# Performance work log

Measured on AMD Instinct MI355X. Metric: run time of the kernel, lower is better.

The kernel has to match this reference:

```python
import jax, jax.numpy as jnp
import numpy as np

B, P, U = 512, 24, 24
IN_T, IN_I, IN_O = 768, 2048, 512
INI = 512            # ini_hidden_dim for all three input linears
H = 1000             # BiLSTM hidden; embed_d = 2*H
E = 2 * H            # embed_d = 2000
INIA = 512           # agg init_linear out dim
HA = 1000            # agg BiLSTM hidden


def _bilstm1(x, W, b):
    """Single-step bidirectional LSTM from zero initial state.
    x: [..., D], W: [2, 4H, D] (fwd/bwd stacked), b: [2, 4H] (b_ih+b_hh).
    With h0=c0=0: gates = x@W_ih^T + b; c = sigmoid(i)*tanh(g); h = sigmoid(o)*tanh(c).
    Returns [..., 2H] (fwd then bwd, matching torch bidirectional concat)."""
    g = jnp.einsum('...d,khd->...kh', x, W) + b          # [..., 2, 4H]
    i, f, gg, o = jnp.split(g, 4, axis=-1)
    c = jax.nn.sigmoid(i) * jnp.tanh(gg)
    h = jax.nn.sigmoid(o) * jnp.tanh(c)                  # [..., 2, H]
    return h.reshape(h.shape[:-2] + (2 * h.shape[-1],))


def _lin(x, W, b):
    return x @ W.T + b


def setup_inputs() -> dict:
    key = jax.random.key(0)
    ks = iter(jax.random.split(key, 48))
    s = 0.05
    def w(*shape):
        return jax.random.normal(next(ks), shape, jnp.float32) * s
    def dat(*shape):
        return jax.random.normal(next(ks), shape, jnp.float32)
    inp = {
        'c_text': dat(B, IN_T), 'c_image': dat(B, IN_I),
        'p_text': dat(B, P, IN_T), 'p_image': dat(B, P, IN_I),
        'u_text': dat(B, U, IN_T), 'u_other': dat(B, U, IN_O),
        # shared per-type input linears
        'W_lt': w(INI, IN_T), 'b_lt': w(INI),
        'W_li': w(INI, IN_I), 'b_li': w(INI),
        'W_lo': w(INI, IN_O), 'b_lo': w(INI),
        # per-type BiLSTMs (fwd/bwd stacked on axis 0)
        'lstm_t_W': w(2, 4 * H, INI), 'lstm_t_b': w(2, 4 * H),
        'lstm_i_W': w(2, 4 * H, INI), 'lstm_i_b': w(2, 4 * H),
        'lstm_o_W': w(2, 4 * H, INI), 'lstm_o_b': w(2, 4 * H),
        # SameType_Agg stacks (user and post)
        'ua_lin_W': w(INIA, E), 'ua_lin_b': w(INIA),
        'ua_lstm_W': w(2, 4 * HA, INIA), 'ua_lstm_b': w(2, 4 * HA),
        'ua_out_W': w(E, 2 * HA), 'ua_out_b': w(E),
        'pa_lin_W': w(INIA, E), 'pa_lin_b': w(INIA),
        'pa_lstm_W': w(2, 4 * HA, INIA), 'pa_lstm_b': w(2, 4 * HA),
        'pa_out_W': w(E, 2 * HA), 'pa_out_b': w(E),
        # attention vector for post-type center nodes
        'p_att': w(2 * E, 1),
    }
    return inp


def reference(c_text, c_image, p_text, p_image, u_text, u_other,
              W_lt, b_lt, W_li, b_li, W_lo, b_lo,
              lstm_t_W, lstm_t_b, lstm_i_W, lstm_i_b, lstm_o_W, lstm_o_b,
              ua_lin_W, ua_lin_b, ua_lstm_W, ua_lstm_b, ua_out_W, ua_out_b,
              pa_lin_W, pa_lin_b, pa_lstm_W, pa_lstm_b, pa_out_W, pa_out_b,
              p_att):
    def post_birnn(text, image):
        # cat along seq dim of two len-1 outputs then mean over seq == average
        ht = _bilstm1(_lin(text, W_lt, b_lt), lstm_t_W, lstm_t_b)
        hi = _bilstm1(_lin(image, W_li, b_li), lstm_i_W, lstm_i_b)
        return 0.5 * (ht + hi)                            # [..., E]

    def user_birnn(text, other):
        ht = _bilstm1(_lin(text, W_lt, b_lt), lstm_t_W, lstm_t_b)
        ho = _bilstm1(_lin(other, W_lo, b_lo), lstm_o_W, lstm_o_b)
        return 0.5 * (ht + ho)

    def same_type_agg(ce, lW, lb, sW, sb, oW, ob):
        h = _bilstm1(_lin(ce, lW, lb), sW, sb)            # [B, N, 2*HA]
        out = _lin(h, oW, ob)                             # [B, N, E]
        return out.mean(axis=1)                           # mean over neighbors

    c = post_birnn(c_text, c_image)                       # [B, E] (center = post)
    u_agg = same_type_agg(user_birnn(u_text, u_other),
                          ua_lin_W, ua_lin_b, ua_lstm_W, ua_lstm_b, ua_out_W, ua_out_b)
    p_agg = same_type_agg(post_birnn(p_text, p_image),
                          pa_lin_W, pa_lin_b, pa_lstm_W, pa_lstm_b, pa_out_W, pa_out_b)

    pairs = jnp.stack([jnp.concatenate([c, c], -1),
                       jnp.concatenate([c, u_agg], -1),
                       jnp.concatenate([c, p_agg], -1)], axis=1)   # [B, 3, 2E]
    att = jax.nn.leaky_relu(pairs @ p_att, 0.01)          # [B, 3, 1]
    wts = jax.nn.softmax(att, axis=1)[..., 0]             # [B, 3]
    emb3 = jnp.stack([c, u_agg, p_agg], axis=1)           # [B, 3, E]
    return jnp.einsum('bk,bke->be', wts, emb3)            # [B, E]
```

## Files before the change

kernel.cpp:

```cpp
#include <hip/hip_runtime.h>
#include <hip/hip_bf16.h>


typedef __hip_bfloat16 bf16;
typedef __attribute__((ext_vector_type(8))) short short8;
typedef __attribute__((ext_vector_type(4))) float f32x4;

__device__ __forceinline__ float bf2f(bf16 x){ return __bfloat162float(x); }
__device__ __forceinline__ bf16  f2bf(float x){ return __float2bfloat16(x); }

__device__ __forceinline__ void gld16(const bf16* g, bf16* l){
  __builtin_amdgcn_global_load_lds(
      (const __attribute__((address_space(1))) void*)g,
      (__attribute__((address_space(3))) void*)l, 16, 0, 0);
}

__device__ __forceinline__ float sigm(float x){ return 1.0f/(1.0f + __expf(-x)); }
__device__ __forceinline__ float tanhfast(float x){
  x = fminf(fmaxf(x, -15.f), 15.f);
  float e = __expf(2.f*x);
  return (e-1.f)/(e+1.f);
}

struct CvtPtrs { const float* p[25]; };
__constant__ long CVT_CUM[26] = {0, 98304, 98432, 360576, 360704, 426240,
  426368, 1450368, 1452368, 2476368, 2478368, 3502368, 3504368, 3760368,
  3760496, 4784496, 4786496, 5786496, 5786996, 6042996, 6043124, 7067124,
  7069124, 8069124, 8069624, 8070624};

__global__ __launch_bounds__(256) void cvt_all(CvtPtrs P, bf16* __restrict__ arena)
{
  long g = (long)blockIdx.x * 256 + threadIdx.x;
  if (g >= 8070624l) return;
  int lo = 0, hi = 24;
  while (lo < hi) { int mid = (lo + hi + 1) >> 1; if (g >= CVT_CUM[mid]) lo = mid; else hi = mid - 1; }
  long rel = (g - CVT_CUM[lo]) * 4;
  float4 v = *(const float4*)(P.p[lo] + rel);
  union { bf16 h[4]; uint2 u; } t;
  t.h[0]=f2bf(v.x); t.h[1]=f2bf(v.y); t.h[2]=f2bf(v.z); t.h[3]=f2bf(v.w);
  *(uint2*)(arena + CVT_CUM[lo]*4 + rel) = t.u;
}

__global__ __launch_bounds__(256) void gemm_linA32(
    const float* __restrict__ A, const float* __restrict__ A2, int splitx,
    const bf16* __restrict__ Bt, const bf16* __restrict__ bias,
    bf16* __restrict__ C, int M, int N, int K, int lda, int ldb, int ldc)
{
  __shared__ bf16 sm[(128+128)*32];
  bf16* As = sm; bf16* Bs = sm + 128*32;
  const int tid  = threadIdx.x;
  const int wave = tid >> 6, lane = tid & 63;
  const int wr = (wave >> 1) * 64, wc = (wave & 1) * 64;
  const int ln = lane & 15, lq = lane >> 4;
  const long m0 = (long)blockIdx.x * 128;
  const int  n0 = blockIdx.y * 128;

  const float* Abase; long mrow;
  if ((int)blockIdx.x < splitx) { Abase = A;  mrow = m0; }
  else { Abase = A2; mrow = (long)((int)blockIdx.x - splitx) * 128; }

  const int arow = tid >> 1, ahalf = (tid & 1) * 16;
  const float* pA = Abase + (mrow + arow) * (long)lda + ahalf;
  bf16* dA = As + arow * 32 + ahalf;
  const int ch = (tid & 3) * 8;
  int colA = n0 + (tid >> 2);       colA = (colA < N) ? colA : (N - 1);
  int colB = n0 + (tid >> 2) + 64;  colB = (colB < N) ? colB : (N - 1);
  const bf16* pB0 = Bt + (long)colA * ldb + ch;
  const bf16* pB1 = Bt + (long)colB * ldb + ch;
  bf16* dB0 = Bs + tid * 8;
  bf16* dB1 = Bs + (tid + 256) * 8;

  f32x4 acc[4][4] = {};
  for (int ks = 0; ks < (K >> 5); ++ks) {
    __syncthreads();
    {
      float4 v0 = *(const float4*)(pA);
      float4 v1 = *(const float4*)(pA + 4);
      float4 v2 = *(const float4*)(pA + 8);
      float4 v3 = *(const float4*)(pA + 12);
      union { bf16 h[16]; short8 q[2]; } u;
      u.h[0]=f2bf(v0.x); u.h[1]=f2bf(v0.y); u.h[2]=f2bf(v0.z); u.h[3]=f2bf(v0.w);
      u.h[4]=f2bf(v1.x); u.h[5]=f2bf(v1.y); u.h[6]=f2bf(v1.z); u.h[7]=f2bf(v1.w);
      u.h[8]=f2bf(v2.x); u.h[9]=f2bf(v2.y); u.h[10]=f2bf(v2.z); u.h[11]=f2bf(v2.w);
      u.h[12]=f2bf(v3.x); u.h[13]=f2bf(v3.y); u.h[14]=f2bf(v3.z); u.h[15]=f2bf(v3.w);
      *(short8*)(dA)     = u.q[0];
      *(short8*)(dA + 8) = u.q[1];
    }
    gld16(pB0, dB0);
    gld16(pB1, dB1);
    __syncthreads();
    short8 af[4], bv[4];
#pragma unroll
    for (int i = 0; i < 4; ++i)
      af[i] = *(const short8*)(As + (wr + i*16 + ln) * 32 + lq * 8);
#pragma unroll
    for (int j = 0; j < 4; ++j)
      bv[j] = *(const short8*)(Bs + (wc + j*16 + ln) * 32 + lq * 8);
#pragma unroll
    for (int i = 0; i < 4; ++i)
#pragma unroll
      for (int j = 0; j < 4; ++j)
        acc[i][j] = __builtin_amdgcn_mfma_f32_16x16x32_bf16(af[i], bv[j], acc[i][j], 0, 0, 0);
    pA += 32; pB0 += 32; pB1 += 32;
  }
#pragma unroll
  for (int j = 0; j < 4; ++j) {
    int n = n0 + wc + j * 16 + ln;
    if (n < N) {
      float bvv = bf2f(bias[n]);
#pragma unroll
      for (int i = 0; i < 4; ++i)
#pragma unroll
        for (int r = 0; r < 4; ++r) {
          long m = m0 + wr + i * 16 + lq * 4 + r;
          C[m * ldc + n] = f2bf(acc[i][j][r] + bvv);
        }
    } else if (n < ldc) {
#pragma unroll
      for (int i = 0; i < 4; ++i)
#pragma unroll
        for (int r = 0; r < 4; ++r) {
          long m = m0 + wr + i * 16 + lq * 4 + r;
          C[m * ldc + n] = f2bf(0.f);
        }
    }
  }
}

__global__ __launch_bounds__(256) void gemm_lin(
    const bf16* __restrict__ A, const bf16* __restrict__ Bt,
    const bf16* __restrict__ bias, bf16* __restrict__ C,
    int M, int N, int K, int lda, int ldb, int ldc)
{
  __shared__ bf16 sm[(128+128)*32];
  bf16* As = sm; bf16* Bs = sm + 128*32;
  const int tid  = threadIdx.x;
  const int wave = tid >> 6, lane = tid & 63;
  const int wr = (wave >> 1) * 64, wc = (wave & 1) * 64;
  const int ln = lane & 15, lq = lane >> 4;
  const long m0 = (long)blockIdx.x * 128;
  const int  n0 = blockIdx.y * 128;

  const int ch = (tid & 3) * 8;
  const bf16* pA0 = A + (m0 + (tid >> 2)) * (long)lda + ch;
  const bf16* pA1 = A + (m0 + (tid >> 2) + 64) * (long)lda + ch;
  bf16* dA0 = As + tid * 8;
  bf16* dA1 = As + (tid + 256) * 8;
  int colA = n0 + (tid >> 2);       colA = (colA < N) ? colA : (N - 1);
  int colB = n0 + (tid >> 2) + 64;  colB = (colB < N) ? colB : (N - 1);
  const bf16* pB0 = Bt + (long)colA * ldb + ch;
  const bf16* pB1 = Bt + (long)colB * ldb + ch;
  bf16* dB0 = Bs + tid * 8;
  bf16* dB1 = Bs + (tid + 256) * 8;

  f32x4 acc[4][4] = {};
  const int ksteps = (K + 31) >> 5;
  for (int ks = 0; ks < ksteps; ++ks) {
    __syncthreads();
    gld16(pA0, dA0);
    gld16(pA1, dA1);
    gld16(pB0, dB0);
    gld16(pB1, dB1);
    __syncthreads();
    short8 af[4], bv[4];
#pragma unroll
    for (int i = 0; i < 4; ++i)
      af[i] = *(const short8*)(As + (wr + i*16 + ln) * 32 + lq * 8);
#pragma unroll
    for (int j = 0; j < 4; ++j)
      bv[j] = *(const short8*)(Bs + (wc + j*16 + ln) * 32 + lq * 8);
#pragma unroll
    for (int i = 0; i < 4; ++i)
#pragma unroll
      for (int j = 0; j < 4; ++j)
        acc[i][j] = __builtin_amdgcn_mfma_f32_16x16x32_bf16(af[i], bv[j], acc[i][j], 0, 0, 0);
    pA0 += 32; pA1 += 32; pB0 += 32; pB1 += 32;
  }
#pragma unroll
  for (int j = 0; j < 4; ++j) {
    int n = n0 + wc + j * 16 + ln;
    if (n < N) {
      float bvv = bf2f(bias[n]);
#pragma unroll
      for (int i = 0; i < 4; ++i)
#pragma unroll
        for (int r = 0; r < 4; ++r) {
          long m = m0 + wr + i * 16 + lq * 4 + r;
          C[m * ldc + n] = f2bf(acc[i][j][r] + bvv);
        }
    } else if (n < ldc) {
#pragma unroll
      for (int i = 0; i < 4; ++i)
#pragma unroll
        for (int r = 0; r < 4; ++r) {
          long m = m0 + wr + i * 16 + lq * 4 + r;
          C[m * ldc + n] = f2bf(0.f);
        }
    }
  }
}

__global__ __launch_bounds__(256) void gemm_out_f32(
    const bf16* __restrict__ A0, const bf16* __restrict__ A1,
    const bf16* __restrict__ B0, const bf16* __restrict__ B1,
    const bf16* __restrict__ b0, const bf16* __restrict__ b1,
    float* __restrict__ C0, float* __restrict__ C1)
{
  __shared__ bf16 sm[(128+128)*32];
  bf16* As = sm; bf16* Bs = sm + 128*32;
  const int tid  = threadIdx.x;
  const int wave = tid >> 6, lane = tid & 63;
  const int wr = (wave >> 1) * 64, wc = (wave & 1) * 64;
  const int ln = lane & 15, lq = lane >> 4;
  const int seg = blockIdx.x >> 2;
  const long m0 = (long)(blockIdx.x & 3) * 128;
  const int  n0 = blockIdx.y * 128;
  const int N = 2000, lda = 2016, ldb = 2000, ldc = 2000;

  const bf16* A    = seg ? A1 : A0;
  const bf16* Bt   = seg ? B1 : B0;
  const bf16* bias = seg ? b1 : b0;
  float*      C    = seg ? C1 : C0;

  const int ch = (tid & 3) * 8;
  const bf16* pA0 = A + (m0 + (tid >> 2)) * (long)lda + ch;
  const bf16* pA1 = A + (m0 + (tid >> 2) + 64) * (long)lda + ch;
  bf16* dA0 = As + tid * 8;
  bf16* dA1 = As + (tid + 256) * 8;
  int colA = n0 + (tid >> 2);       colA = (colA < N) ? colA : (N - 1);
  int colB = n0 + (tid >> 2) + 64;  colB = (colB < N) ? colB : (N - 1);
  const bf16* pB0 = Bt + (long)colA * ldb + ch;
  const bf16* pB1 = Bt + (long)colB * ldb + ch;
  bf16* dB0 = Bs + tid * 8;
  bf16* dB1 = Bs + (tid + 256) * 8;

  f32x4 acc[4][4] = {};
  for (int ks = 0; ks < 63; ++ks) {
    __syncthreads();
    gld16(pA0, dA0);
    gld16(pA1, dA1);
    gld16(pB0, dB0);
    gld16(pB1, dB1);
    __syncthreads();
    short8 af[4], bv[4];
#pragma unroll
    for (int i = 0; i < 4; ++i)
      af[i] = *(const short8*)(As + (wr + i*16 + ln) * 32 + lq * 8);
#pragma unroll
    for (int j = 0; j < 4; ++j)
      bv[j] = *(const short8*)(Bs + (wc + j*16 + ln) * 32 + lq * 8);
#pragma unroll
    for (int i = 0; i < 4; ++i)
#pragma unroll
      for (int j = 0; j < 4; ++j)
        acc[i][j] = __builtin_amdgcn_mfma_f32_16x16x32_bf16(af[i], bv[j], acc[i][j], 0, 0, 0);
    pA0 += 32; pA1 += 32; pB0 += 32; pB1 += 32;
  }
#pragma unroll
  for (int j = 0; j < 4; ++j) {
    int n = n0 + wc + j * 16 + ln;
    if (n < N) {
      float bvv = bf2f(bias[n]);
#pragma unroll
      for (int i = 0; i < 4; ++i)
#pragma unroll
        for (int r = 0; r < 4; ++r) {
          long m = m0 + wr + i * 16 + lq * 4 + r;
          C[m * ldc + n] = acc[i][j][r] + bvv;
        }
    }
  }
}

__global__ __launch_bounds__(256) void gemm_lstm(
    const bf16* __restrict__ A, const bf16* __restrict__ W,
    const bf16* __restrict__ bvec, const bf16* __restrict__ other,
    bf16* __restrict__ Hout, int ldo, int ldc, int combine)
{
  __shared__ bf16 sm[(128+96)*32];
  bf16* As = sm; bf16* Bs = sm + 128*32;
  const int tid  = threadIdx.x;
  const int wave = tid >> 6, lane = tid & 63;
  const int wr = (wave >> 1) * 64, wc = (wave & 1) * 48;
  const int ln = lane & 15, lq = lane >> 4;
  const long m0 = (long)blockIdx.x * 128;
  const int dir = blockIdx.y >> 5, jb = blockIdx.y & 31;

  const int ch = (tid & 3) * 8;
  const bf16* pA0 = A + (m0 + (tid >> 2)) * 512 + ch;
  const bf16* pA1 = A + (m0 + (tid >> 2) + 64) * 512 + ch;
  bf16* dA0 = As + tid * 8;
  bf16* dA1 = As + (tid + 256) * 8;
  auto brow = [&](int t) -> long {
    int tc = t >> 2;
    int grp = tc / 48, wi = tc % 48, cf = wi >> 4;
    int jj = jb * 32 + grp * 16 + (wi & 15);
    jj = (jj < 1000) ? jj : 999;
    return (long)(dir * 4000 + cf * 1000 + (cf ? 1000 : 0) + jj);
  };
  const bf16* pB0 = W + brow(tid) * 512 + ch;
  const bf16* pB1 = W + brow(tid + 256) * 512 + ch;
  bf16* dB0 = Bs + tid * 8;
  bf16* dB1 = Bs + (tid + 256) * 8;
  const bool doB1 = (tid < 128);

  f32x4 acc[4][3] = {};
  for (int ks = 0; ks < 16; ++ks) {
    __syncthreads();
    gld16(pA0, dA0);
    gld16(pA1, dA1);
    gld16(pB0, dB0);
    if (doB1) gld16(pB1, dB1);
    __syncthreads();
    short8 af[4], bv[3];
#pragma unroll
    for (int i = 0; i < 4; ++i)
      af[i] = *(const short8*)(As + (wr + i*16 + ln) * 32 + lq * 8);
#pragma unroll
    for (int j = 0; j < 3; ++j)
      bv[j] = *(const short8*)(Bs + (wc + j*16 + ln) * 32 + lq * 8);
#pragma unroll
    for (int i = 0; i < 4; ++i)
#pragma unroll
      for (int j = 0; j < 3; ++j)
        acc[i][j] = __builtin_amdgcn_mfma_f32_16x16x32_bf16(af[i], bv[j], acc[i][j], 0, 0, 0);
    pA0 += 32; pA1 += 32; pB0 += 32; pB1 += 32;
  }
  const int jj  = jb * 32 + (wave & 1) * 16 + ln;
  const int jc  = (jj < 1000) ? jj : 999;
  const float bI = bf2f(bvec[dir * 4000 + jc]);
  const float bG = bf2f(bvec[dir * 4000 + 2000 + jc]);
  const float bO = bf2f(bvec[dir * 4000 + 3000 + jc]);
  const int col = dir * 1000 + jj;
  const bool sv = (jj < 1000);
  const bool sz = (!sv) && (dir == 1) && (col < ldc);
  if (!sv && !sz) return;
#pragma unroll
  for (int i = 0; i < 4; ++i)
#pragma unroll
    for (int r = 0; r < 4; ++r) {
      long m = m0 + wr + i * 16 + lq * 4 + r;
      float h = 0.f;
      if (sv) {
        float gi = acc[i][0][r] + bI;
        float gg = acc[i][1][r] + bG;
        float go = acc[i][2][r] + bO;
        float cc = sigm(gi) * tanhfast(gg);
        h = sigm(go) * tanhfast(cc);
        if (combine) h = 0.5f * (h + bf2f(other[m * ldo + col]));
      }
      Hout[m * ldc + col] = f2bf(h);
    }
}

__global__ __launch_bounds__(256) void meanh(const bf16* __restrict__ X, bf16* __restrict__ Y)
{
  long idx = (long)blockIdx.x * 256 + threadIdx.x;
  if (idx >= 512l * 2016) return;
  long b = idx / 2016, e = idx % 2016;
  const bf16* p = X + b * 24 * 2016 + e;
  float s = 0.f;
#pragma unroll
  for (int n = 0; n < 24; ++n) s += bf2f(p[(long)n * 2016]);
  Y[idx] = f2bf(s * (1.f / 24.f));
}

__global__ __launch_bounds__(256) void attn_mix(
    const bf16* __restrict__ Cm, const float* __restrict__ U,
    const float* __restrict__ P, const float* __restrict__ att,
    float* __restrict__ out, int ldcm)
{
  const int b = blockIdx.x, tid = threadIdx.x;
  __shared__ float red[4][4];
  __shared__ float wsh[3];
  float s0 = 0, s1 = 0, s2 = 0, s3 = 0;
  const long baseC = (long)b * ldcm;
  const long base  = (long)b * 2000;
  for (int e = tid; e < 2000; e += 256) {
    float cv = bf2f(Cm[baseC + e]);
    float al = att[e];
    float ah = att[2000 + e];
    s0 += cv * al; s1 += cv * ah;
    s2 += U[base + e] * ah; s3 += P[base + e] * ah;
  }
#pragma unroll
  for (int o = 32; o; o >>= 1) {
    s0 += __shfl_down(s0, o); s1 += __shfl_down(s1, o);
    s2 += __shfl_down(s2, o); s3 += __shfl_down(s3, o);
  }
  if ((tid & 63) == 0) {
    int w = tid >> 6;
    red[w][0] = s0; red[w][1] = s1; red[w][2] = s2; red[w][3] = s3;
  }
  __syncthreads();
  if (tid == 0) {
    float a0 = 0, a1 = 0, a2 = 0, a3 = 0;
    for (int w = 0; w < 4; ++w) { a0 += red[w][0]; a1 += red[w][1]; a2 += red[w][2]; a3 += red[w][3]; }
    float t0 = a0 + a1, t1 = a0 + a2, t2 = a0 + a3;
    t0 = t0 > 0 ? t0 : 0.01f * t0;
    t1 = t1 > 0 ? t1 : 0.01f * t1;
    t2 = t2 > 0 ? t2 : 0.01f * t2;
    float mx = fmaxf(t0, fmaxf(t1, t2));
    float e0 = __expf(t0 - mx), e1 = __expf(t1 - mx), e2 = __expf(t2 - mx);
    float inv = 1.f / (e0 + e1 + e2);
    wsh[0] = e0 * inv; wsh[1] = e1 * inv; wsh[2] = e2 * inv;
  }
  __syncthreads();
  float w0 = wsh[0], w1 = wsh[1], w2 = wsh[2];
  for (int e = tid; e < 2000; e += 256)
    out[base + e] = w0 * bf2f(Cm[baseC + e]) + w1 * U[base + e] + w2 * P[base + e];
}

extern "C" void kernel_launch(void* const* d_in, const int* in_sizes, int n_in,
                              void* d_out, int out_size, void* d_ws, size_t ws_size,
                              hipStream_t stream)
{
  const float* c_text  = (const float*)d_in[0];
  const float* c_image = (const float*)d_in[1];
  const float* p_text  = (const float*)d_in[2];
  const float* p_image = (const float*)d_in[3];
  const float* u_text  = (const float*)d_in[4];
  const float* u_other = (const float*)d_in[5];
  const float* p_att   = (const float*)d_in[30];
  float* out = (float*)d_out;

  char* ws = (char*)d_ws;
  size_t off = 0;
  auto alloc = [&](size_t bytes) -> char* {
    char* p = ws + off; off += (bytes + 255) & ~(size_t)255; return p;
  };
  bf16* ARENA = (bf16*)alloc(32282496ull * 2);
  bf16* BIG1  = (bf16*)alloc(12800ull * 2016 * 2);
  bf16* BIG2  = (bf16*)alloc(12800ull * 2016 * 2);
  bf16* X1    = (bf16*)alloc(12800ull * 512 * 2);
  bf16* X2    = (bf16*)alloc(12800ull * 512 * 2);
  bf16* Yu    = (bf16*)alloc(512ull * 2016 * 2);
  bf16* Yp    = (bf16*)alloc(512ull * 2016 * 2);
  float* UA   = (float*)alloc(512ull * 2000 * 4);
  float* PA   = (float*)alloc(512ull * 2000 * 4);
  (void)ws_size; (void)in_sizes; (void)n_in; (void)out_size;

  const bf16* aW_lt = ARENA + 0;        const bf16* ab_lt = ARENA + 393216;
  const bf16* aW_li = ARENA + 393728;   const bf16* ab_li = ARENA + 1442304;
  const bf16* aW_lo = ARENA + 1442816;  const bf16* ab_lo = ARENA + 1704960;
  const bf16* alt_W = ARENA + 1705472;  const bf16* alt_b = ARENA + 5801472;
  const bf16* ali_W = ARENA + 5809472;  const bf16* ali_b = ARENA + 9905472;
  const bf16* alo_W = ARENA + 9913472;  const bf16* alo_b = ARENA + 14009472;
  const bf16* aua_lin_W  = ARENA + 14017472; const bf16* aua_lin_b  = ARENA + 15041472;
  const bf16* aua_lstm_W = ARENA + 15041984; const bf16* aua_lstm_b = ARENA + 19137984;
  const bf16* aua_out_W  = ARENA + 19145984; const bf16* aua_out_b  = ARENA + 23145984;
  const bf16* apa_lin_W  = ARENA + 23147984; const bf16* apa_lin_b  = ARENA + 24171984;
  const bf16* apa_lstm_W = ARENA + 24172496; const bf16* apa_lstm_b = ARENA + 28268496;
  const bf16* apa_out_W  = ARENA + 28276496; const bf16* apa_out_b  = ARENA + 32276496;

  CvtPtrs cp;
  for (int i = 0; i < 25; ++i) cp.p[i] = (const float*)d_in[6 + i];
  cvt_all<<<dim3(31527), dim3(256), 0, stream>>>(cp, ARENA);

  dim3 blk(256);
  const int NOSPLIT = 1 << 30;

  gemm_linA32<<<dim3(96,4), blk, 0, stream>>>(u_text,  u_text,  NOSPLIT, aW_lt, ab_lt, X1, 12288, 512, 768, 768, 768, 512);
  gemm_linA32<<<dim3(96,4), blk, 0, stream>>>(u_other, u_other, NOSPLIT, aW_lo, ab_lo, X2, 12288, 512, 512, 512, 512, 512);
  gemm_lstm<<<dim3(96,64), blk, 0, stream>>>(X1, alt_W, alt_b, nullptr, BIG1, 2016, 2016, 0);
  gemm_lstm<<<dim3(96,64), blk, 0, stream>>>(X2, alo_W, alo_b, BIG1,    BIG2, 2016, 2016, 1);
  gemm_lin<<<dim3(96,4), blk, 0, stream>>>(BIG2, aua_lin_W, aua_lin_b, X1, 12288, 512, 2000, 2016, 2000, 512);
  gemm_lstm<<<dim3(96,64), blk, 0, stream>>>(X1, aua_lstm_W, aua_lstm_b, nullptr, BIG1, 2016, 2016, 0);
  meanh<<<dim3(4032), blk, 0, stream>>>(BIG1, Yu);

  gemm_linA32<<<dim3(100,4), blk, 0, stream>>>(p_text,  c_text,  96, aW_lt, ab_lt, X1, 12800, 512, 768,  768,  768,  512);
  gemm_linA32<<<dim3(100,4), blk, 0, stream>>>(p_image, c_image, 96, aW_li, ab_li, X2, 12800, 512, 2048, 2048, 2048, 512);
  gemm_lstm<<<dim3(100,64), blk, 0, stream>>>(X1, alt_W, alt_b, nullptr, BIG1, 2016, 2016, 0);
  gemm_lstm<<<dim3(100,64), blk, 0, stream>>>(X2, ali_W, ali_b, BIG1,    BIG2, 2016, 2016, 1);
  gemm_lin<<<dim3(96,4), blk, 0, stream>>>(BIG2, apa_lin_W, apa_lin_b, X1, 12288, 512, 2000, 2016, 2000, 512);
  gemm_lstm<<<dim3(96,64), blk, 0, stream>>>(X1, apa_lstm_W, apa_lstm_b, nullptr, BIG1, 2016, 2016, 0);
  meanh<<<dim3(4032), blk, 0, stream>>>(BIG1, Yp);

  gemm_out_f32<<<dim3(8,16), blk, 0, stream>>>(Yu, Yp, aua_out_W, apa_out_W,
                                               aua_out_b, apa_out_b, UA, PA);
  attn_mix<<<dim3(512), blk, 0, stream>>>(BIG2 + 12288l * 2016, UA, PA, p_att, out, 2016);
}
```

Before: 1.571 ms.

## Double-buffer LDS tiles in all GEMM kernels to overlap loads with MFMA

```diff
diff --git a/kernel.cpp b/kernel.cpp
--- a/kernel.cpp
+++ b/kernel.cpp
@@ -46,8 +46,7 @@
     const bf16* __restrict__ Bt, const bf16* __restrict__ bias,
     bf16* __restrict__ C, int M, int N, int K, int lda, int ldb, int ldc)
 {
-  __shared__ bf16 sm[(128+128)*32];
-  bf16* As = sm; bf16* Bs = sm + 128*32;
+  __shared__ bf16 sm[2][(128+128)*32];
   const int tid  = threadIdx.x;
   const int wave = tid >> 6, lane = tid & 63;
   const int wr = (wave >> 1) * 64, wc = (wave & 1) * 64;
@@ -61,34 +60,53 @@
 
   const int arow = tid >> 1, ahalf = (tid & 1) * 16;
   const float* pA = Abase + (mrow + arow) * (long)lda + ahalf;
-  bf16* dA = As + arow * 32 + ahalf;
+  const int sAoff = arow * 32 + ahalf;
   const int ch = (tid & 3) * 8;
   int colA = n0 + (tid >> 2);       colA = (colA < N) ? colA : (N - 1);
   int colB = n0 + (tid >> 2) + 64;  colB = (colB < N) ? colB : (N - 1);
   const bf16* pB0 = Bt + (long)colA * ldb + ch;
   const bf16* pB1 = Bt + (long)colB * ldb + ch;
-  bf16* dB0 = Bs + tid * 8;
-  bf16* dB1 = Bs + (tid + 256) * 8;
+  const int sB0 = 128*32 + tid * 8, sB1 = 128*32 + (tid + 256) * 8;
+
+  auto cvtA = [&](bf16* dst, float4 v0, float4 v1, float4 v2, float4 v3){
+    union { bf16 h[16]; short8 q[2]; } u;
+    u.h[0]=f2bf(v0.x); u.h[1]=f2bf(v0.y); u.h[2]=f2bf(v0.z); u.h[3]=f2bf(v0.w);
+    u.h[4]=f2bf(v1.x); u.h[5]=f2bf(v1.y); u.h[6]=f2bf(v1.z); u.h[7]=f2bf(v1.w);
+    u.h[8]=f2bf(v2.x); u.h[9]=f2bf(v2.y); u.h[10]=f2bf(v2.z); u.h[11]=f2bf(v2.w);
+    u.h[12]=f2bf(v3.x); u.h[13]=f2bf(v3.y); u.h[14]=f2bf(v3.z); u.h[15]=f2bf(v3.w);
+    *(short8*)(dst)     = u.q[0];
+    *(short8*)(dst + 8) = u.q[1];
+  };
+
+  const int ksteps = K >> 5;
+  {
+    float4 v0 = *(const float4*)(pA);
+    float4 v1 = *(const float4*)(pA + 4);
+    float4 v2 = *(const float4*)(pA + 8);
+    float4 v3 = *(const float4*)(pA + 12);
+    cvtA(sm[0] + sAoff, v0, v1, v2, v3);
+    gld16(pB0, sm[0] + sB0);
+    gld16(pB1, sm[0] + sB1);
+    pA += 32; pB0 += 32; pB1 += 32;
+  }
+  __syncthreads();
 
   f32x4 acc[4][4] = {};
-  for (int ks = 0; ks < (K >> 5); ++ks) {
-    __syncthreads();
-    {
-      float4 v0 = *(const float4*)(pA);
-      float4 v1 = *(const float4*)(pA + 4);
-      float4 v2 = *(const float4*)(pA + 8);
-      float4 v3 = *(const float4*)(pA + 12);
-      union { bf16 h[16]; short8 q[2]; } u;
-      u.h[0]=f2bf(v0.x); u.h[1]=f2bf(v0.y); u.h[2]=f2bf(v0.z); u.h[3]=f2bf(v0.w);
-      u.h[4]=f2bf(v1.x); u.h[5]=f2bf(v1.y); u.h[6]=f2bf(v1.z); u.h[7]=f2bf(v1.w);
-      u.h[8]=f2bf(v2.x); u.h[9]=f2bf(v2.y); u.h[10]=f2bf(v2.z); u.h[11]=f2bf(v2.w);
-      u.h[12]=f2bf(v3.x); u.h[13]=f2bf(v3.y); u.h[14]=f2bf(v3.z); u.h[15]=f2bf(v3.w);
-      *(short8*)(dA)     = u.q[0];
-      *(short8*)(dA + 8) = u.q[1];
-    }
-    gld16(pB0, dB0);
-    gld16(pB1, dB1);
-    __syncthreads();
+  for (int ks = 0; ks < ksteps; ++ks) {
+    const bf16* S = sm[ks & 1];
+    bf16* Sn = sm[(ks + 1) & 1];
+    const bool stage = (ks + 1 < ksteps);
+    float4 v0, v1, v2, v3;
+    if (stage) {
+      v0 = *(const float4*)(pA);
+      v1 = *(const float4*)(pA + 4);
+      v2 = *(const float4*)(pA + 8);
+      v3 = *(const float4*)(pA + 12);
+      gld16(pB0, Sn + sB0);
+      gld16(pB1, Sn + sB1);
+      pA += 32; pB0 += 32; pB1 += 32;
+    }
+    const bf16* As = S; const bf16* Bs = S + 128*32;
     short8 af[4], bv[4];
 #pragma unroll
     for (int i = 0; i < 4; ++i)
@@ -101,7 +119,8 @@
 #pragma unroll
       for (int j = 0; j < 4; ++j)
         acc[i][j] = __builtin_amdgcn_mfma_f32_16x16x32_bf16(af[i], bv[j], acc[i][j], 0, 0, 0);
-    pA += 32; pB0 += 32; pB1 += 32;
+    if (stage) cvtA(Sn + sAoff, v0, v1, v2, v3);
+    __syncthreads();
   }
 #pragma unroll
   for (int j = 0; j < 4; ++j) {
@@ -132,8 +151,7 @@
     const bf16* __restrict__ bias, bf16* __restrict__ C,
     int M, int N, int K, int lda, int ldb, int ldc)
 {
-  __shared__ bf16 sm[(128+128)*32];
-  bf16* As = sm; bf16* Bs = sm + 128*32;
+  __shared__ bf16 sm[2][(128+128)*32];
   const int tid  = threadIdx.x;
   const int wave = tid >> 6, lane = tid & 63;
   const int wr = (wave >> 1) * 64, wc = (wave & 1) * 64;
@@ -144,24 +162,31 @@
   const int ch = (tid & 3) * 8;
   const bf16* pA0 = A + (m0 + (tid >> 2)) * (long)lda + ch;
   const bf16* pA1 = A + (m0 + (tid >> 2) + 64) * (long)lda + ch;
-  bf16* dA0 = As + tid * 8;
-  bf16* dA1 = As + (tid + 256) * 8;
   int colA = n0 + (tid >> 2);       colA = (colA < N) ? colA : (N - 1);
   int colB = n0 + (tid >> 2) + 64;  colB = (colB < N) ? colB : (N - 1);
   const bf16* pB0 = Bt + (long)colA * ldb + ch;
   const bf16* pB1 = Bt + (long)colB * ldb + ch;
-  bf16* dB0 = Bs + tid * 8;
-  bf16* dB1 = Bs + (tid + 256) * 8;
+  const int sA0 = tid * 8, sA1 = (tid + 256) * 8;
+  const int sB0 = 128*32 + tid * 8, sB1 = 128*32 + (tid + 256) * 8;
+
+  const int ksteps = (K + 31) >> 5;
+  {
+    gld16(pA0, sm[0] + sA0); gld16(pA1, sm[0] + sA1);
+    gld16(pB0, sm[0] + sB0); gld16(pB1, sm[0] + sB1);
+    pA0 += 32; pA1 += 32; pB0 += 32; pB1 += 32;
+  }
+  __syncthreads();
 
   f32x4 acc[4][4] = {};
-  const int ksteps = (K + 31) >> 5;
   for (int ks = 0; ks < ksteps; ++ks) {
-    __syncthreads();
-    gld16(pA0, dA0);
-    gld16(pA1, dA1);
-    gld16(pB0, dB0);
-    gld16(pB1, dB1);
-    __syncthreads();
+    const bf16* S = sm[ks & 1];
+    bf16* Sn = sm[(ks + 1) & 1];
+    if (ks + 1 < ksteps) {
+      gld16(pA0, Sn + sA0); gld16(pA1, Sn + sA1);
+      gld16(pB0, Sn + sB0); gld16(pB1, Sn + sB1);
+      pA0 += 32; pA1 += 32; pB0 += 32; pB1 += 32;
+    }
+    const bf16* As = S; const bf16* Bs = S + 128*32;
     short8 af[4], bv[4];
 #pragma unroll
     for (int i = 0; i < 4; ++i)
@@ -174,7 +199,7 @@
 #pragma unroll
       for (int j = 0; j < 4; ++j)
         acc[i][j] = __builtin_amdgcn_mfma_f32_16x16x32_bf16(af[i], bv[j], acc[i][j], 0, 0, 0);
-    pA0 += 32; pA1 += 32; pB0 += 32; pB1 += 32;
+    __syncthreads();
   }
 #pragma unroll
   for (int j = 0; j < 4; ++j) {
@@ -206,8 +231,7 @@
     const bf16* __restrict__ b0, const bf16* __restrict__ b1,
     float* __restrict__ C0, float* __restrict__ C1)
 {
-  __shared__ bf16 sm[(128+128)*32];
-  bf16* As = sm; bf16* Bs = sm + 128*32;
+  __shared__ bf16 sm[2][(128+128)*32];
   const int tid  = threadIdx.x;
   const int wave = tid >> 6, lane = tid & 63;
   const int wr = (wave >> 1) * 64, wc = (wave & 1) * 64;
@@ -225,23 +249,30 @@
   const int ch = (tid & 3) * 8;
   const bf16* pA0 = A + (m0 + (tid >> 2)) * (long)lda + ch;
   const bf16* pA1 = A + (m0 + (tid >> 2) + 64) * (long)lda + ch;
-  bf16* dA0 = As + tid * 8;
-  bf16* dA1 = As + (tid + 256) * 8;
   int colA = n0 + (tid >> 2);       colA = (colA < N) ? colA : (N - 1);
   int colB = n0 + (tid >> 2) + 64;  colB = (colB < N) ? colB : (N - 1);
   const bf16* pB0 = Bt + (long)colA * ldb + ch;
   const bf16* pB1 = Bt + (long)colB * ldb + ch;
-  bf16* dB0 = Bs + tid * 8;
-  bf16* dB1 = Bs + (tid + 256) * 8;
+  const int sA0 = tid * 8, sA1 = (tid + 256) * 8;
+  const int sB0 = 128*32 + tid * 8, sB1 = 128*32 + (tid + 256) * 8;
+
+  {
+    gld16(pA0, sm[0] + sA0); gld16(pA1, sm[0] + sA1);
+    gld16(pB0, sm[0] + sB0); gld16(pB1, sm[0] + sB1);
+    pA0 += 32; pA1 += 32; pB0 += 32; pB1 += 32;
+  }
+  __syncthreads();
 
   f32x4 acc[4][4] = {};
   for (int ks = 0; ks < 63; ++ks) {
-    __syncthreads();
-    gld16(pA0, dA0);
-    gld16(pA1, dA1);
-    gld16(pB0, dB0);
-    gld16(pB1, dB1);
-    __syncthreads();
+    const bf16* S = sm[ks & 1];
+    bf16* Sn = sm[(ks + 1) & 1];
+    if (ks + 1 < 63) {
+      gld16(pA0, Sn + sA0); gld16(pA1, Sn + sA1);
+      gld16(pB0, Sn + sB0); gld16(pB1, Sn + sB1);
+      pA0 += 32; pA1 += 32; pB0 += 32; pB1 += 32;
+    }
+    const bf16* As = S; const bf16* Bs = S + 128*32;
     short8 af[4], bv[4];
 #pragma unroll
     for (int i = 0; i < 4; ++i)
@@ -254,7 +285,7 @@
 #pragma unroll
       for (int j = 0; j < 4; ++j)
         acc[i][j] = __builtin_amdgcn_mfma_f32_16x16x32_bf16(af[i], bv[j], acc[i][j], 0, 0, 0);
-    pA0 += 32; pA1 += 32; pB0 += 32; pB1 += 32;
+    __syncthreads();
   }
 #pragma unroll
   for (int j = 0; j < 4; ++j) {
@@ -277,8 +308,7 @@
     const bf16* __restrict__ bvec, const bf16* __restrict__ other,
     bf16* __restrict__ Hout, int ldo, int ldc, int combine)
 {
-  __shared__ bf16 sm[(128+96)*32];
-  bf16* As = sm; bf16* Bs = sm + 128*32;
+  __shared__ bf16 sm[2][(128+96)*32];
   const int tid  = threadIdx.x;
   const int wave = tid >> 6, lane = tid & 63;
   const int wr = (wave >> 1) * 64, wc = (wave & 1) * 48;
@@ -289,8 +319,6 @@
   const int ch = (tid & 3) * 8;
   const bf16* pA0 = A + (m0 + (tid >> 2)) * 512 + ch;
   const bf16* pA1 = A + (m0 + (tid >> 2) + 64) * 512 + ch;
-  bf16* dA0 = As + tid * 8;
-  bf16* dA1 = As + (tid + 256) * 8;
   auto brow = [&](int t) -> long {
     int tc = t >> 2;
     int grp = tc / 48, wi = tc % 48, cf = wi >> 4;
@@ -300,18 +328,29 @@
   };
   const bf16* pB0 = W + brow(tid) * 512 + ch;
   const bf16* pB1 = W + brow(tid + 256) * 512 + ch;
-  bf16* dB0 = Bs + tid * 8;
-  bf16* dB1 = Bs + (tid + 256) * 8;
+  const int sA0 = tid * 8, sA1 = (tid + 256) * 8;
+  const int sB0 = 128*32 + tid * 8, sB1 = 128*32 + (tid + 256) * 8;
   const bool doB1 = (tid < 128);
+
+  {
+    gld16(pA0, sm[0] + sA0); gld16(pA1, sm[0] + sA1);
+    gld16(pB0, sm[0] + sB0);
+    if (doB1) gld16(pB1, sm[0] + sB1);
+    pA0 += 32; pA1 += 32; pB0 += 32; pB1 += 32;
+  }
+  __syncthreads();
 
   f32x4 acc[4][3] = {};
   for (int ks = 0; ks < 16; ++ks) {
-    __syncthreads();
-    gld16(pA0, dA0);
-    gld16(pA1, dA1);
-    gld16(pB0, dB0);
-    if (doB1) gld16(pB1, dB1);
-    __syncthreads();
+    const bf16* S = sm[ks & 1];
+    bf16* Sn = sm[(ks + 1) & 1];
+    if (ks + 1 < 16) {
+      gld16(pA0, Sn + sA0); gld16(pA1, Sn + sA1);
+      gld16(pB0, Sn + sB0);
+      if (doB1) gld16(pB1, Sn + sB1);
+      pA0 += 32; pA1 += 32; pB0 += 32; pB1 += 32;
+    }
+    const bf16* As = S; const bf16* Bs = S + 128*32;
     short8 af[4], bv[3];
 #pragma unroll
     for (int i = 0; i < 4; ++i)
@@ -324,7 +363,7 @@
 #pragma unroll
       for (int j = 0; j < 3; ++j)
         acc[i][j] = __builtin_amdgcn_mfma_f32_16x16x32_bf16(af[i], bv[j], acc[i][j], 0, 0, 0);
-    pA0 += 32; pA1 += 32; pB0 += 32; pB1 += 32;
+    __syncthreads();
   }
   const int jj  = jb * 32 + (wave & 1) * 16 + ln;
   const int jc  = (jj < 1000) ? jj : 999;
```

Result: faster. 1.495 ms (-4.8%).
